# Kernel tuning notes

Measured on AMD Instinct MI355X. Metric: run time of the kernel, lower is better.

## Reference

```python
import jax, jax.numpy as jnp
import numpy as np

B, N, D, H, QK, HID = 4, 1024, 1024, 16, 64, 4096
BETA = 1.0 / float(np.sqrt(QK))  # default attn_beta = 1/sqrt(qk_dim)


def setup_inputs() -> dict:
    key = jax.random.key(0)
    k1, k2, k3, k4 = jax.random.split(key, 4)
    x = jax.random.normal(k1, (B, N, D), dtype=jnp.float32)
    scale = 1.0 / float(np.sqrt(D))
    Wq = jax.random.normal(k2, (H, QK, D), dtype=jnp.float32) * scale
    Wk = jax.random.normal(k3, (H, QK, D), dtype=jnp.float32) * scale
    W_hop = jax.random.normal(k4, (D, HID), dtype=jnp.float32) * scale
    return {"x": x, "Wq": Wq, "Wk": Wk, "W_hop": W_hop}


def _energy(x, Wq, Wk, W_hop):
    # Graph energy attention (dense path, no adjacency / mask)
    q = jnp.einsum('bnd,hqd->bhnq', x, Wq)  # [B,H,N,QK]
    k = jnp.einsum('bnd,hqd->bhnq', x, Wk)  # [B,H,N,QK]
    scores = BETA * jnp.einsum('bhnq,bhmq->bhnm', q, k)  # [B,H,N,N]
    e_attn = -(1.0 / BETA) * jnp.sum(jax.nn.logsumexp(scores, axis=-1))
    # Hopfield energy: -1/2 * sum relu(x W)^2
    h = jax.nn.relu(jnp.einsum('bnd,de->bne', x, W_hop))  # [B,N,HID]
    e_hop = -0.5 * jnp.sum(h * h)
    return e_attn + e_hop


def reference(x, Wq, Wk, W_hop):
    # Module returns (grad of energy w.r.t. x, energy) via grad_and_value
    energy, grad = jax.value_and_grad(_energy, argnums=0)(x, Wq, Wk, W_hop)
    return grad, energy
```

## Files before the change

### kernel.cpp

```cpp
#include <hip/hip_runtime.h>
#include <hip/hip_bf16.h>
#include <math.h>

#define BETA 0.125f
#define INV_BETA 8.0f

typedef __attribute__((ext_vector_type(8))) short short8v;
typedef __attribute__((ext_vector_type(4))) float f32x4;
typedef union { short8v v; unsigned short u[8]; } v8u;

#define OFF_XB   0u
#define OFF_WCB  2097152u
#define OFF_WCTB 3145728u
#define OFF_WHB  4194304u
#define OFF_WHTB 6291456u
#define OFF_H    8388608u
#define OFF_QB   16777216u
#define OFF_KB   18874368u
#define OFF_QT   20971520u
#define OFF_KT   23068672u
#define OFF_DQK  25165824u
#define OFF_LSE  29360128u
#define OFF_PL   29425664u
#define OFF_PH   29429760u

__device__ __forceinline__ unsigned short f2b(float f) {
    unsigned u = __float_as_uint(f);
    return (unsigned short)((u + 0x7fffu + ((u >> 16) & 1u)) >> 16);
}

__device__ __forceinline__ void gload_lds16(const unsigned short* g, void* l) {
    __builtin_amdgcn_global_load_lds(
        (const __attribute__((address_space(1))) unsigned int*)g,
        (__attribute__((address_space(3))) unsigned int*)l, 16, 0, 0);
}

__device__ __forceinline__ void xcd_swz(int n, int gx, int& bx, int& by) {
    int id = blockIdx.x;
    int nid = (id & 7) * (n >> 3) + (id >> 3);
    bx = nid % gx;
    by = nid / gx;
}

__global__ __launch_bounds__(256) void k_prep(const float* __restrict__ x,
                                              const float* __restrict__ Wq,
                                              const float* __restrict__ Wk,
                                              const float* __restrict__ Whop,
                                              unsigned short* __restrict__ XB,
                                              unsigned short* __restrict__ WCB,
                                              unsigned short* __restrict__ WHB,
                                              unsigned short* __restrict__ WCTB,
                                              unsigned short* __restrict__ WHTB) {
    __shared__ float t[32][33];
    int id = blockIdx.x;
    int tid = threadIdx.x;
    if (id < 10240) {
        int i = id * 256 + tid;
        const float* s;
        unsigned short* d;
        int j;
        if (i < 1048576) { s = x; d = XB; j = i; }
        else if (i < 1310720) { s = Wq; d = WCB; j = i - 1048576; }
        else if (i < 1572864) { s = Wk; d = WCB + 1048576; j = i - 1310720; }
        else { s = Whop; d = WHB; j = i - 1572864; }
        float4 v = ((const float4*)s)[j];
        ushort4 o;
        o.x = f2b(v.x); o.y = f2b(v.y); o.z = f2b(v.z); o.w = f2b(v.w);
        ((ushort4*)d)[j] = o;
        return;
    }
    int id2 = id - 10240;
    int bx = id2 % 192;
    int byy = id2 / 192;
    int tx = tid & 31, ty = tid >> 5;
    if (bx < 64) {
        int j0 = bx * 32, d0 = byy * 32;
#pragma unroll
        for (int i = 0; i < 4; ++i) {
            int j = j0 + ty + 8 * i;
            const float* src = (j < 1024) ? (Wq + (size_t)j * 1024) : (Wk + (size_t)(j - 1024) * 1024);
            t[ty + 8 * i][tx] = src[d0 + tx];
        }
        __syncthreads();
#pragma unroll
        for (int i = 0; i < 4; ++i)
            WCTB[(size_t)(d0 + ty + 8 * i) * 2048 + j0 + tx] = f2b(t[tx][ty + 8 * i]);
    } else {
        int e0 = (bx - 64) * 32, d0 = byy * 32;
#pragma unroll
        for (int i = 0; i < 4; ++i)
            t[ty + 8 * i][tx] = Whop[(size_t)(d0 + ty + 8 * i) * 4096 + e0 + tx];
        __syncthreads();
#pragma unroll
        for (int i = 0; i < 4; ++i)
            WHTB[(size_t)(e0 + ty + 8 * i) * 1024 + d0 + tx] = f2b(t[tx][ty + 8 * i]);
    }
}

template <int MI, int NJ>
__device__ __forceinline__ void gemm_core(const unsigned short* __restrict__ A, int lda,
                                          const unsigned short* __restrict__ Bm, int ldb,
                                          int kdim, int rowBase, int colBase,
                                          unsigned short* ldsA, unsigned short* ldsB,
                                          f32x4 (&acc)[MI][NJ]) {
    const int tid = threadIdx.x, lane = tid & 63;
    const int wv = tid >> 6;
    const int lr = lane & 15, lg = lane >> 4;
    const int wrow = (wv >> 1) * (MI * 16);
    const int wcol = (wv & 1) * (NJ * 16);

    for (int kk = 0; kk < kdim; kk += 64) {
#pragma unroll
        for (int iss = 0; iss < MI; ++iss) {
            int p = iss * 256 + tid;
            int row = p >> 3, c = p & 7, cs = c ^ (row & 7);
            gload_lds16(&A[(size_t)(rowBase + row) * lda + kk + cs * 8], (char*)ldsA + p * 16);
        }
#pragma unroll
        for (int iss = 0; iss < NJ; ++iss) {
            int p = iss * 256 + tid;
            int row = p >> 3, c = p & 7, cs = c ^ (row & 7);
            gload_lds16(&Bm[(size_t)(colBase + row) * ldb + kk + cs * 8], (char*)ldsB + p * 16);
        }
        __syncthreads();
#pragma unroll
        for (int kc = 0; kc < 2; ++kc) {
            short8v av[MI], bv[NJ];
#pragma unroll
            for (int i = 0; i < MI; ++i) {
                int row = wrow + i * 16 + lr;
                av[i] = *(const short8v*)((const char*)ldsA + row * 128 + ((kc * 4 + lg) ^ (row & 7)) * 16);
            }
#pragma unroll
            for (int j = 0; j < NJ; ++j) {
                int row = wcol + j * 16 + lr;
                bv[j] = *(const short8v*)((const char*)ldsB + row * 128 + ((kc * 4 + lg) ^ (row & 7)) * 16);
            }
#pragma unroll
            for (int i = 0; i < MI; ++i)
#pragma unroll
                for (int j = 0; j < NJ; ++j)
                    acc[i][j] = __builtin_amdgcn_mfma_f32_16x16x32_bf16(av[i], bv[j], acc[i][j], 0, 0, 0);
        }
        __syncthreads();
    }
}

#define GEMM_IDX(MI, NJ, BX, BY)                                                 \
    const int tid = threadIdx.x, lane = tid & 63, wv = tid >> 6;                 \
    const int lr = lane & 15, lg = lane >> 4;                                    \
    const int row0 = (BX) * (MI * 32) + (wv >> 1) * (MI * 16);                   \
    const int col0 = (BY) * (NJ * 32) + (wv & 1) * (NJ * 16);                    \
    f32x4 acc[MI][NJ];                                                           \
    _Pragma("unroll") for (int i = 0; i < MI; ++i)                               \
        _Pragma("unroll") for (int j = 0; j < NJ; ++j)                           \
            acc[i][j] = (f32x4){0.f, 0.f, 0.f, 0.f};

__global__ __launch_bounds__(256) void mm_proj(const unsigned short* __restrict__ XB,
                                               const unsigned short* __restrict__ WCB,
                                               unsigned short* __restrict__ Qb,
                                               unsigned short* __restrict__ Kb) {
    __shared__ unsigned short ldsA[64 * 64];
    __shared__ unsigned short ldsB[128 * 64];
    int bx, by;
    xcd_swz(1024, 64, bx, by);
    GEMM_IDX(2, 4, bx, by)
    gemm_core<2, 4>(XB, 1024, WCB, 1024, 1024, bx * 64, by * 128, ldsA, ldsB, acc);
    unsigned short* dst = (col0 < 1024) ? Qb : Kb;
    const int cbase = col0 & 1023;
#pragma unroll
    for (int i = 0; i < 2; ++i)
#pragma unroll
        for (int r = 0; r < 4; ++r) {
            int rg = row0 + i * 16 + lg * 4 + r;
            int bb = rg >> 10, n = rg & 1023;
#pragma unroll
            for (int j = 0; j < 4; ++j) {
                int c = cbase + j * 16 + lr;
                int h = c >> 6, q = c & 63;
                dst[((size_t)(bb * 16 + h) * 1024 + n) * 64 + q] = f2b(acc[i][j][r]);
            }
        }
}

__global__ __launch_bounds__(256) void mm_hopfwd(const unsigned short* __restrict__ XB,
                                                 const unsigned short* __restrict__ WHTB,
                                                 unsigned short* __restrict__ Hn,
                                                 float* __restrict__ PH) {
    __shared__ unsigned short ldsA[128 * 64];
    __shared__ unsigned short ldsB[128 * 64];
    __shared__ float red[4];
    int bx, by;
    xcd_swz(1024, 32, bx, by);
    GEMM_IDX(4, 4, bx, by)
    gemm_core<4, 4>(XB, 1024, WHTB, 1024, 1024, bx * 128, by * 128, ldsA, ldsB, acc);
    float ss = 0.f;
#pragma unroll
    for (int i = 0; i < 4; ++i)
#pragma unroll
        for (int r = 0; r < 4; ++r) {
            size_t rg = row0 + i * 16 + lg * 4 + r;
#pragma unroll
            for (int j = 0; j < 4; ++j) {
                float hv = fmaxf(acc[i][j][r], 0.f);
                ss += hv * hv;
                Hn[rg * 4096 + col0 + j * 16 + lr] = f2b(-hv);
            }
        }
#pragma unroll
    for (int off = 32; off; off >>= 1) ss += __shfl_down(ss, off);
    if (lane == 0) red[wv] = ss;
    __syncthreads();
    if (tid == 0) PH[blockIdx.x] = red[0] + red[1] + red[2] + red[3];
}

__global__ __launch_bounds__(256) void mm_gradall(const unsigned short* __restrict__ Hn,
                                                  const unsigned short* __restrict__ WHB,
                                                  const unsigned short* __restrict__ DQK,
                                                  const unsigned short* __restrict__ WCTB,
                                                  float* __restrict__ out) {
    __shared__ unsigned short ldsA[64 * 64];
    __shared__ unsigned short ldsB[128 * 64];
    int id = blockIdx.x;
    int nid = (id & 7) * 64 + (id >> 3);
    int by = nid & 7;
    int bx = nid >> 3;
    GEMM_IDX(2, 4, bx, by)
    gemm_core<2, 4>(Hn, 4096, WHB, 4096, 4096, bx * 64, by * 128, ldsA, ldsB, acc);
    gemm_core<2, 4>(DQK, 2048, WCTB, 2048, 2048, bx * 64, by * 128, ldsA, ldsB, acc);
#pragma unroll
    for (int i = 0; i < 2; ++i)
#pragma unroll
        for (int r = 0; r < 4; ++r) {
            size_t rg = row0 + i * 16 + lg * 4 + r;
#pragma unroll
            for (int j = 0; j < 4; ++j)
                out[rg * 1024 + col0 + j * 16 + lr] = acc[i][j][r];
        }
}

__global__ __launch_bounds__(256) void k_tqk(const unsigned short* __restrict__ Qb,
                                             const unsigned short* __restrict__ Kb,
                                             unsigned short* __restrict__ QT,
                                             unsigned short* __restrict__ KT) {
    __shared__ unsigned short T[64][65];
    const int z = blockIdx.z;
    const unsigned short* src = z ? Kb : Qb;
    unsigned short* dst = z ? KT : QT;
    const int bh = blockIdx.y;
    const int n0 = blockIdx.x * 64;
    const int t = threadIdx.x;
    {
        int row = t >> 3;
        int colc = (t & 7) * 8;
#pragma unroll
        for (int ii = 0; ii < 2; ++ii) {
            int r = row + 32 * ii;
            v8u vv;
            vv.v = *(const short8v*)&src[((size_t)(bh << 10) + n0 + r) * 64 + colc];
#pragma unroll
            for (int j = 0; j < 8; ++j) T[r][colc + j] = vv.u[j];
        }
    }
    __syncthreads();
    {
        int q = t >> 2;
        int nc = (t & 3) * 16;
        unsigned short buf[16];
#pragma unroll
        for (int j = 0; j < 16; ++j) buf[j] = T[nc + j][q];
        *(short8v*)&dst[((size_t)bh * 64 + q) * 1024 + n0 + nc] = *(short8v*)&buf[0];
        *(short8v*)&dst[((size_t)bh * 64 + q) * 1024 + n0 + nc + 8] = *(short8v*)&buf[8];
    }
}

__global__ __launch_bounds__(256) void k_dq(const unsigned short* __restrict__ Qb,
                                            const unsigned short* __restrict__ Kb,
                                            const unsigned short* __restrict__ KT,
                                            float* __restrict__ LSE,
                                            float* __restrict__ PL,
                                            unsigned short* __restrict__ DQK) {
    __shared__ unsigned short Ktile[2][64 * 64];
    __shared__ unsigned short Ttile[2][64 * 64];
    __shared__ unsigned short P[4][1024];
    int nt, bh;
    xcd_swz(1024, 16, nt, bh);
    const int tid = threadIdx.x, lane = tid & 63, wv = tid >> 6;
    const int nw = nt * 64 + wv * 16;
    const int lr = lane & 15, lg = lane >> 4;
    unsigned short* Pw = &P[wv][0];

    auto stage = [&](int buf, int m0) {
#pragma unroll
        for (int iss = 0; iss < 2; ++iss) {
            int p = iss * 256 + tid;
            int row = p >> 3, c = p & 7, cs = c ^ (row & 7);
            gload_lds16(&Kb[((size_t)(bh << 10) + m0 + row) * 64 + cs * 8],
                        (char*)&Ktile[buf][0] + p * 16);
            gload_lds16(&KT[((size_t)bh * 64 + row) * 1024 + m0 + cs * 8],
                        (char*)&Ttile[buf][0] + p * 16);
        }
    };

    short8v qa[2];
#pragma unroll
    for (int kc = 0; kc < 2; ++kc)
        qa[kc] = *(const short8v*)&Qb[((size_t)(bh << 10) + nw + lr) * 64 + kc * 32 + lg * 8];

    float sm[4];
    f32x4 dq[4];
#pragma unroll
    for (int r = 0; r < 4; ++r) sm[r] = 0.f;
#pragma unroll
    for (int qb = 0; qb < 4; ++qb) dq[qb] = (f32x4){0.f, 0.f, 0.f, 0.f};

    stage(0, 0);
    __syncthreads();
    int buf = 0;
    for (int mt = 0; mt < 16; ++mt) {
        if (mt < 15) stage(buf ^ 1, (mt + 1) * 64);
        const char* Kt = (const char*)&Ktile[buf][0];
        const char* Tt = (const char*)&Ttile[buf][0];
#pragma unroll
        for (int ct = 0; ct < 4; ++ct) {
            int brow = ct * 16 + lr;
            short8v bk0 = *(const short8v*)(Kt + brow * 128 + ((lg) ^ (brow & 7)) * 16);
            short8v bk1 = *(const short8v*)(Kt + brow * 128 + ((lg + 4) ^ (brow & 7)) * 16);
            f32x4 s = {0.f, 0.f, 0.f, 0.f};
            s = __builtin_amdgcn_mfma_f32_16x16x32_bf16(qa[0], bk0, s, 0, 0, 0);
            s = __builtin_amdgcn_mfma_f32_16x16x32_bf16(qa[1], bk1, s, 0, 0, 0);
#pragma unroll
            for (int r = 0; r < 4; ++r) {
                float p = __expf(s[r] * BETA);
                sm[r] += p;
                int row = lg * 4 + r;
                int off = (row * 64 + ct * 16 + lr) ^ ((row & 7) << 3);
                Pw[off] = f2b(p);
            }
        }
        short8v pa[2];
#pragma unroll
        for (int kc = 0; kc < 2; ++kc) {
            int off = (lr * 64 + kc * 32 + lg * 8) ^ ((lr & 7) << 3);
            pa[kc] = *(const short8v*)&Pw[off];
        }
#pragma unroll
        for (int qb = 0; qb < 4; ++qb) {
            int brow = qb * 16 + lr;
            short8v b0 = *(const short8v*)(Tt + brow * 128 + ((lg) ^ (brow & 7)) * 16);
            short8v b1 = *(const short8v*)(Tt + brow * 128 + ((lg + 4) ^ (brow & 7)) * 16);
            dq[qb] = __builtin_amdgcn_mfma_f32_16x16x32_bf16(pa[0], b0, dq[qb], 0, 0, 0);
            dq[qb] = __builtin_amdgcn_mfma_f32_16x16x32_bf16(pa[1], b1, dq[qb], 0, 0, 0);
        }
        __syncthreads();
        buf ^= 1;
    }

#pragma unroll
    for (int off = 1; off < 16; off <<= 1)
#pragma unroll
        for (int r = 0; r < 4; ++r) sm[r] += __shfl_xor(sm[r], off);

    const int b = bh >> 4, h = bh & 15;
#pragma unroll
    for (int r = 0; r < 4; ++r) {
        float inv = 1.0f / sm[r];
#pragma unroll
        for (int qb = 0; qb < 4; ++qb)
            DQK[((size_t)(b << 10) + nw + lg * 4 + r) * 2048 + h * 64 + qb * 16 + lr] =
                f2b(-dq[qb][r] * inv);
    }

    float lsum = 0.f;
    if (lr == 0) {
#pragma unroll
        for (int r = 0; r < 4; ++r) {
            float l = __logf(sm[r]);
            LSE[(size_t)(bh << 10) + nw + lg * 4 + r] = l;
            lsum += l;
        }
    }
    lsum += __shfl_xor(lsum, 16);
    lsum += __shfl_xor(lsum, 32);
    if (lane == 0) PL[(size_t)blockIdx.x * 4 + wv] = lsum;
}

__global__ __launch_bounds__(256) void k_dk(const unsigned short* __restrict__ Qb,
                                            const unsigned short* __restrict__ Kb,
                                            const unsigned short* __restrict__ QT,
                                            const float* __restrict__ LSE,
                                            unsigned short* __restrict__ DQK) {
    __shared__ unsigned short Qtile[2][64 * 64];
    __shared__ unsigned short Ttile[2][64 * 64];
    __shared__ unsigned short P[4][1024];
    int mt, bh;
    xcd_swz(1024, 16, mt, bh);
    const int tid = threadIdx.x, lane = tid & 63, wv = tid >> 6;
    const int mw = mt * 64 + wv * 16;
    const int lr = lane & 15, lg = lane >> 4;
    unsigned short* Pw = &P[wv][0];

    auto stage = [&](int buf, int n0) {
#pragma unroll
        for (int iss = 0; iss < 2; ++iss) {
            int p = iss * 256 + tid;
            int row = p >> 3, c = p & 7, cs = c ^ (row & 7);
            gload_lds16(&Qb[((size_t)(bh << 10) + n0 + row) * 64 + cs * 8],
                        (char*)&Qtile[buf][0] + p * 16);
            gload_lds16(&QT[((size_t)bh * 64 + row) * 1024 + n0 + cs * 8],
                        (char*)&Ttile[buf][0] + p * 16);
        }
    };

    short8v ka[2];
#pragma unroll
    for (int kc = 0; kc < 2; ++kc)
        ka[kc] = *(const short8v*)&Kb[((size_t)(bh << 10) + mw + lr) * 64 + kc * 32 + lg * 8];

    f32x4 dk[4];
#pragma unroll
    for (int qb = 0; qb < 4; ++qb) dk[qb] = (f32x4){0.f, 0.f, 0.f, 0.f};

    stage(0, 0);
    __syncthreads();
    int buf = 0;
    for (int ntl = 0; ntl < 16; ++ntl) {
        const int n0 = ntl * 64;
        float lse_c[4];
#pragma unroll
        for (int ct = 0; ct < 4; ++ct)
            lse_c[ct] = LSE[(size_t)(bh << 10) + n0 + ct * 16 + lr];
        if (ntl < 15) stage(buf ^ 1, n0 + 64);
        const char* Qt = (const char*)&Qtile[buf][0];
        const char* Tt = (const char*)&Ttile[buf][0];
#pragma unroll
        for (int ct = 0; ct < 4; ++ct) {
            int brow = ct * 16 + lr;
            short8v bq0 = *(const short8v*)(Qt + brow * 128 + ((lg) ^ (brow & 7)) * 16);
            short8v bq1 = *(const short8v*)(Qt + brow * 128 + ((lg + 4) ^ (brow & 7)) * 16);
            f32x4 s = {0.f, 0.f, 0.f, 0.f};
            s = __builtin_amdgcn_mfma_f32_16x16x32_bf16(ka[0], bq0, s, 0, 0, 0);
            s = __builtin_amdgcn_mfma_f32_16x16x32_bf16(ka[1], bq1, s, 0, 0, 0);
#pragma unroll
            for (int r = 0; r < 4; ++r) {
                float p = __expf(s[r] * BETA - lse_c[ct]);
                int row = lg * 4 + r;
                int off = (row * 64 + ct * 16 + lr) ^ ((row & 7) << 3);
                Pw[off] = f2b(p);
            }
        }
        short8v pa[2];
#pragma unroll
        for (int kc = 0; kc < 2; ++kc) {
            int off = (lr * 64 + kc * 32 + lg * 8) ^ ((lr & 7) << 3);
            pa[kc] = *(const short8v*)&Pw[off];
        }
#pragma unroll
        for (int qb = 0; qb < 4; ++qb) {
            int brow = qb * 16 + lr;
            short8v b0 = *(const short8v*)(Tt + brow * 128 + ((lg) ^ (brow & 7)) * 16);
            short8v b1 = *(const short8v*)(Tt + brow * 128 + ((lg + 4) ^ (brow & 7)) * 16);
            dk[qb] = __builtin_amdgcn_mfma_f32_16x16x32_bf16(pa[0], b0, dk[qb], 0, 0, 0);
            dk[qb] = __builtin_amdgcn_mfma_f32_16x16x32_bf16(pa[1], b1, dk[qb], 0, 0, 0);
        }
        __syncthreads();
        buf ^= 1;
    }
    const int b = bh >> 4, h = bh & 15;
#pragma unroll
    for (int qb = 0; qb < 4; ++qb)
#pragma unroll
        for (int r = 0; r < 4; ++r)
            DQK[((size_t)(b << 10) + mw + lg * 4 + r) * 2048 + 1024 + h * 64 + qb * 16 + lr] = f2b(-dk[qb][r]);
}

__global__ __launch_bounds__(256) void k_fin(const float* __restrict__ pl,
                                             const float* __restrict__ ph,
                                             float* __restrict__ out) {
    const int tid = threadIdx.x;
    float s1 = 0.f, s2 = 0.f;
    for (int i = tid; i < 4096; i += 256) s1 += pl[i];
    for (int i = tid; i < 1024; i += 256) s2 += ph[i];
#pragma unroll
    for (int off = 32; off; off >>= 1) {
        s1 += __shfl_down(s1, off);
        s2 += __shfl_down(s2, off);
    }
    __shared__ float r1[4], r2[4];
    if ((tid & 63) == 0) { r1[tid >> 6] = s1; r2[tid >> 6] = s2; }
    __syncthreads();
    if (tid == 0) {
        float S1 = r1[0] + r1[1] + r1[2] + r1[3];
        float S2 = r2[0] + r2[1] + r2[2] + r2[3];
        out[(size_t)4194304] = -INV_BETA * S1 - 0.5f * S2;
    }
}

extern "C" void kernel_launch(void* const* d_in, const int* in_sizes, int n_in,
                              void* d_out, int out_size, void* d_ws, size_t ws_size,
                              hipStream_t stream) {
    (void)in_sizes; (void)n_in; (void)out_size; (void)ws_size;
    const float* x    = (const float*)d_in[0];
    const float* Wq   = (const float*)d_in[1];
    const float* Wk   = (const float*)d_in[2];
    const float* Whop = (const float*)d_in[3];
    float* out = (float*)d_out;
    float* ws = (float*)d_ws;

    unsigned short* XB   = (unsigned short*)(ws + OFF_XB);
    unsigned short* WCB  = (unsigned short*)(ws + OFF_WCB);
    unsigned short* WCTB = (unsigned short*)(ws + OFF_WCTB);
    unsigned short* WHB  = (unsigned short*)(ws + OFF_WHB);
    unsigned short* WHTB = (unsigned short*)(ws + OFF_WHTB);
    unsigned short* Hn   = (unsigned short*)(ws + OFF_H);
    unsigned short* Qb   = (unsigned short*)(ws + OFF_QB);
    unsigned short* Kb   = (unsigned short*)(ws + OFF_KB);
    unsigned short* QT   = (unsigned short*)(ws + OFF_QT);
    unsigned short* KT   = (unsigned short*)(ws + OFF_KT);
    unsigned short* DQK  = (unsigned short*)(ws + OFF_DQK);
    float* LSE = ws + OFF_LSE;
    float* PL  = ws + OFF_PL;
    float* PH  = ws + OFF_PH;

    dim3 blk(256);
    k_prep<<<dim3(16384), blk, 0, stream>>>(x, Wq, Wk, Whop, XB, WCB, WHB, WCTB, WHTB);

    mm_proj<<<dim3(1024), blk, 0, stream>>>(XB, WCB, Qb, Kb);
    k_tqk<<<dim3(16, 64, 2), blk, 0, stream>>>(Qb, Kb, QT, KT);
    k_dq<<<dim3(1024), blk, 0, stream>>>(Qb, Kb, KT, LSE, PL, DQK);
    k_dk<<<dim3(1024), blk, 0, stream>>>(Qb, Kb, QT, LSE, DQK);

    mm_hopfwd<<<dim3(1024), blk, 0, stream>>>(XB, WHTB, Hn, PH);
    mm_gradall<<<dim3(512), blk, 0, stream>>>(Hn, WHB, DQK, WCTB, out);
    k_fin<<<dim3(1), blk, 0, stream>>>(PL, PH, out);
}
```

Baseline: 331.7 us.

## Rewrite Hopfield forward GEMM with 256x256 tiles and double-buffered LDS pipeline

Replaces the generic 128x128 gemm_core call in mm_hopfwd with a custom 512-thread kernel computing 256x256 output tiles. It uses double-buffered LDS, staged in quarter chunks interleaved with the MFMA work and raised wave priority during MFMA. The larger tile increases operand reuse and cuts global traffic, and the async prefetch overlaps loads with compute. In exchange it uses 128KB of LDS and a 128-float accumulator per thread, which limits occupancy to one block per CU and launches only 256 blocks. The final reduction in k_fin is adjusted to read the 256 partial sums.

```diff
diff --git a/kernel.cpp b/kernel.cpp
--- a/kernel.cpp
+++ b/kernel.cpp
@@ -183,35 +183,109 @@
         }
 }
 
-__global__ __launch_bounds__(256) void mm_hopfwd(const unsigned short* __restrict__ XB,
+__global__ __launch_bounds__(512) void mm_hopfwd(const unsigned short* __restrict__ XB,
                                                  const unsigned short* __restrict__ WHTB,
                                                  unsigned short* __restrict__ Hn,
                                                  float* __restrict__ PH) {
-    __shared__ unsigned short ldsA[128 * 64];
-    __shared__ unsigned short ldsB[128 * 64];
-    __shared__ float red[4];
-    int bx, by;
-    xcd_swz(1024, 32, bx, by);
-    GEMM_IDX(4, 4, bx, by)
-    gemm_core<4, 4>(XB, 1024, WHTB, 1024, 1024, bx * 128, by * 128, ldsA, ldsB, acc);
+    __shared__ unsigned short ldsA[2][256 * 64];
+    __shared__ unsigned short ldsB[2][256 * 64];
+    __shared__ float red[8];
+    const int tid = threadIdx.x, lane = tid & 63, wv = tid >> 6;
+    const int lr = lane & 15, lg = lane >> 4;
+    const int wm = wv >> 2, wn = wv & 3;
+    int id = blockIdx.x;
+    int nid = (id & 7) * 32 + (id >> 3);
+    int bx = nid & 15, by = nid >> 4;
+    const int rowB = bx * 256, colB = by * 256;
+
+    f32x4 acc[8][4];
+#pragma unroll
+    for (int i = 0; i < 8; ++i)
+#pragma unroll
+        for (int j = 0; j < 4; ++j) acc[i][j] = (f32x4){0.f, 0.f, 0.f, 0.f};
+
+    auto stageh = [&](int h, int tstep, int bufi) {
+        const bool isB = (h & 1) != 0;
+        const int half = h >> 1;
+        const unsigned short* gsrc = isB ? WHTB : XB;
+        const int gbase = (isB ? colB : rowB) + half * 128;
+        char* ldst = (char*)(isB ? &ldsB[bufi][0] : &ldsA[bufi][0]) + half * 16384;
+        const int kk = tstep * 64;
+#pragma unroll
+        for (int iss = 0; iss < 2; ++iss) {
+            int p = iss * 512 + tid;
+            int row = p >> 3, c = p & 7, cs = c ^ (row & 7);
+            gload_lds16(&gsrc[(size_t)(gbase + row) * 1024 + kk + cs * 8], ldst + p * 16);
+        }
+    };
+
+    stageh(0, 0, 0); stageh(1, 0, 0); stageh(2, 0, 0); stageh(3, 0, 0);
+    asm volatile("s_waitcnt vmcnt(0)" ::: "memory");
+    asm volatile("s_barrier" ::: "memory");
+
+    for (int t = 0; t < 16; ++t) {
+        const int cur = t & 1;
+        const char* bufA = (const char*)&ldsA[cur][0] + wm * 16384;
+        const char* bufB = (const char*)&ldsB[cur][0] + (wn >> 1) * 16384;
+        const int bloc = (wn & 1) * 64;
+#pragma unroll
+        for (int q = 0; q < 4; ++q) {
+            const int qm = q >> 1, qn = q & 1;
+            if (t + 1 < 16) stageh(q, t + 1, cur ^ 1);
+            if (q == 0) asm volatile("s_waitcnt vmcnt(2)" ::: "memory");
+            asm volatile("s_barrier" ::: "memory");
+            short8v av[4][2], bv[2][2];
+#pragma unroll
+            for (int m2 = 0; m2 < 4; ++m2) {
+                int lrow = (qm * 4 + m2) * 16 + lr;
+#pragma unroll
+                for (int kc = 0; kc < 2; ++kc)
+                    av[m2][kc] = *(const short8v*)(bufA + lrow * 128 + (((kc * 4 + lg) ^ (lrow & 7)) * 16));
+            }
+#pragma unroll
+            for (int n2 = 0; n2 < 2; ++n2) {
+                int lrow = bloc + (qn * 2 + n2) * 16 + lr;
+#pragma unroll
+                for (int kc = 0; kc < 2; ++kc)
+                    bv[n2][kc] = *(const short8v*)(bufB + lrow * 128 + (((kc * 4 + lg) ^ (lrow & 7)) * 16));
+            }
+            __builtin_amdgcn_s_setprio(1);
+#pragma unroll
+            for (int m2 = 0; m2 < 4; ++m2)
+#pragma unroll
+                for (int n2 = 0; n2 < 2; ++n2)
+#pragma unroll
+                    for (int kc = 0; kc < 2; ++kc)
+                        acc[qm * 4 + m2][qn * 2 + n2] = __builtin_amdgcn_mfma_f32_16x16x32_bf16(
+                            av[m2][kc], bv[n2][kc], acc[qm * 4 + m2][qn * 2 + n2], 0, 0, 0);
+            __builtin_amdgcn_s_setprio(0);
+            asm volatile("s_barrier" ::: "memory");
+        }
+    }
+
     float ss = 0.f;
 #pragma unroll
-    for (int i = 0; i < 4; ++i)
+    for (int mf = 0; mf < 8; ++mf)
 #pragma unroll
         for (int r = 0; r < 4; ++r) {
-            size_t rg = row0 + i * 16 + lg * 4 + r;
-#pragma unroll
-            for (int j = 0; j < 4; ++j) {
-                float hv = fmaxf(acc[i][j][r], 0.f);
+            size_t rg = rowB + wm * 128 + mf * 16 + lg * 4 + r;
+#pragma unroll
+            for (int nf = 0; nf < 4; ++nf) {
+                float hv = fmaxf(acc[mf][nf][r], 0.f);
                 ss += hv * hv;
-                Hn[rg * 4096 + col0 + j * 16 + lr] = f2b(-hv);
+                Hn[rg * 4096 + colB + wn * 64 + nf * 16 + lr] = f2b(-hv);
             }
         }
 #pragma unroll
     for (int off = 32; off; off >>= 1) ss += __shfl_down(ss, off);
     if (lane == 0) red[wv] = ss;
     __syncthreads();
-    if (tid == 0) PH[blockIdx.x] = red[0] + red[1] + red[2] + red[3];
+    if (tid == 0) {
+        float s = 0.f;
+#pragma unroll
+        for (int w = 0; w < 8; ++w) s += red[w];
+        PH[blockIdx.x] = s;
+    }
 }
 
 __global__ __launch_bounds__(256) void mm_gradall(const unsigned short* __restrict__ Hn,
@@ -480,7 +554,7 @@
     const int tid = threadIdx.x;
     float s1 = 0.f, s2 = 0.f;
     for (int i = tid; i < 4096; i += 256) s1 += pl[i];
-    for (int i = tid; i < 1024; i += 256) s2 += ph[i];
+    if (tid < 256) s2 = ph[tid];
 #pragma unroll
     for (int off = 32; off; off >>= 1) {
         s1 += __shfl_down(s1, off);
@@ -530,7 +604,7 @@
     k_dq<<<dim3(1024), blk, 0, stream>>>(Qb, Kb, KT, LSE, PL, DQK);
     k_dk<<<dim3(1024), blk, 0, stream>>>(Qb, Kb, QT, LSE, DQK);
 
-    mm_hopfwd<<<dim3(1024), blk, 0, stream>>>(XB, WHTB, Hn, PH);
+    mm_hopfwd<<<dim3(256), dim3(512), 0, stream>>>(XB, WHTB, Hn, PH);
     mm_gradall<<<dim3(512), blk, 0, stream>>>(Hn, WHB, DQK, WCTB, out);
     k_fin<<<dim3(1), blk, 0, stream>>>(PL, PH, out);
 }
```

New measurement: 325.6 us. No clear change (-1.9%).
